# Kernel tuning notes

Hardware: AMD Instinct MI355X
Metric: run time of the kernel (lower is better)

The kernel has to match this reference:

```python
import jax, jax.numpy as jnp
import numpy as np

IN_SIZE = 512
OUT_SIZE = 256
HIDDEN = 256
LN_EPS = 1e-5


def setup_inputs() -> dict:
    key = jax.random.key(0)
    ks = jax.random.split(key, 9)
    B, S, K = 8, 2048, 16
    net_in = jax.random.normal(ks[0], (B, S, K, IN_SIZE), dtype=jnp.float32)
    embeds = jax.random.normal(ks[1], (B, S, OUT_SIZE), dtype=jnp.float32)
    m = jax.random.uniform(ks[2], (B, S, K, 1), dtype=jnp.float32)
    W1 = jax.random.normal(ks[3], (IN_SIZE, HIDDEN), dtype=jnp.float32) * 0.02
    b1 = jnp.full((HIDDEN,), 0.02, dtype=jnp.float32)
    Wf = jax.random.normal(ks[4], (HIDDEN, OUT_SIZE + 1), dtype=jnp.float32) * 0.02
    bf = jnp.zeros((OUT_SIZE + 1,), dtype=jnp.float32)
    gamma = jnp.ones((OUT_SIZE,), dtype=jnp.float32)
    beta = jnp.zeros((OUT_SIZE,), dtype=jnp.float32)
    return {"net_in": net_in, "embeds": embeds, "m": m, "W1": W1, "b1": b1,
            "Wf": Wf, "bf": bf, "gamma": gamma, "beta": beta}


def reference(net_in, embeds, m, W1, b1, Wf, bf, gamma, beta):
    # MLP: one hidden relu layer, final linear to out_size+1
    h = jax.nn.relu(jnp.einsum('bski,ih->bskh', net_in, W1) + b1)
    out = jnp.einsum('bskh,ho->bsko', h, Wf) + bf          # [B,S,K,out+1]
    # sigmoid on last channel (link weight), then mask
    out = jnp.concatenate([out[..., :-1], jax.nn.sigmoid(out[..., -1:])], axis=-1)
    out = m * out
    link_weight = out[..., -1] + 1e-8                       # [B,S,K]
    norm = jnp.sum(link_weight, axis=2, keepdims=True)      # [B,S,1]
    weights = (link_weight / norm)[..., None]               # [B,S,K,1]
    updates = jnp.sum(out * weights, axis=2)                # [B,S,out+1]
    # residual update
    upd_weights = updates[..., -1:]
    embeds_new = embeds + upd_weights * updates[..., :-1]
    # LayerNorm over last dim
    mu = jnp.mean(embeds_new, axis=-1, keepdims=True)
    var = jnp.var(embeds_new, axis=-1, keepdims=True)
    return (embeds_new - mu) * jax.lax.rsqrt(var + LN_EPS) * gamma + beta
```

## Files before the change

### kernel.cpp

```cpp
#include <hip/hip_runtime.h>

typedef short s16x8 __attribute__((ext_vector_type(8)));
typedef float f32x4 __attribute__((ext_vector_type(4)));

__device__ __forceinline__ unsigned short f2bf(float f) {
    union { float f; unsigned u; } v; v.f = f;
    return (unsigned short)((v.u + 0x7FFFu + ((v.u >> 16) & 1u)) >> 16);
}
__device__ __forceinline__ float bf2f(unsigned short h) {
    union { unsigned u; float f; } v; v.u = ((unsigned)h) << 16;
    return v.f;
}

__device__ __forceinline__ void wg_barrier_lds() {
    __builtin_amdgcn_sched_barrier(0);
    asm volatile("s_waitcnt lgkmcnt(0)" ::: "memory");
    __builtin_amdgcn_s_barrier();
    __builtin_amdgcn_sched_barrier(0);
}

#define NBLK 1024

__global__ void prep_weights(const float* __restrict__ W1, const float* __restrict__ Wf,
                             unsigned short* __restrict__ W1T, unsigned short* __restrict__ WfT) {
    int t = blockIdx.x * 256 + threadIdx.x;
    {
        int c  = t >> 13;
        int n  = (t >> 5) & 255;
        int kk = t & 31;
        W1T[t] = f2bf(W1[(c * 32 + kk) * 256 + n]);
    }
    if (t < 65536) {
        int c  = t >> 13;
        int n  = (t >> 5) & 255;
        int hh = t & 31;
        WfT[t] = f2bf(Wf[(c * 32 + hh) * 257 + n]);
    }
}

__global__ __launch_bounds__(1024)
void fused_embed(const float* __restrict__ net_in, const float* __restrict__ embeds,
                 const float* __restrict__ mg, const float* __restrict__ W1,
                 const float* __restrict__ b1, const float* __restrict__ Wf,
                 const float* __restrict__ bfv, const float* __restrict__ gam,
                 const float* __restrict__ bet, float* __restrict__ out,
                 const unsigned short* __restrict__ W1T, const unsigned short* __restrict__ WfT)
{
    __shared__ unsigned short Abuf[2][256][32];
    __shared__ unsigned short Hbuf[128][260];
    __shared__ unsigned short gbuf[16][264];
    __shared__ float updb[16][264];
    __shared__ float sbuf[16];

    const int tid  = threadIdx.x;
    const int lane = tid & 63;
    const int wid  = tid >> 6;
    const int wr   = wid >> 2;
    const int wc   = wid & 3;
    const int l15  = lane & 15;
    const int g8   = (lane >> 4) * 8;
    const int blk  = blockIdx.x;
    const int row0 = blk * 256;

    const f32x4 zero4 = {0.f, 0.f, 0.f, 0.f};

    f32x4 acc[4][4];
    #pragma unroll
    for (int i = 0; i < 4; ++i)
        #pragma unroll
        for (int j = 0; j < 4; ++j)
            acc[i][j] = zero4;

    const int ar = tid >> 2;
    const int ac = (tid & 3) * 8;
    const int wbase = (wc * 64 + l15) * 32 + g8;

    float4 vaA[2], vbA[2];

#define A_ISSUE(KC, S) do { \
        const float* _src = &net_in[(row0 + ar) * 512 + (KC) * 32 + ac]; \
        vaA[S] = *(const float4*)_src; \
        vbA[S] = *(const float4*)(_src + 4); \
    } while (0)

#define A_WRITE(KC, S) do { \
        int4 _pk; \
        asm("v_cvt_pk_bf16_f32 %0, %1, %2" : "=v"(_pk.x) : "v"(vaA[S].x), "v"(vaA[S].y)); \
        asm("v_cvt_pk_bf16_f32 %0, %1, %2" : "=v"(_pk.y) : "v"(vaA[S].z), "v"(vaA[S].w)); \
        asm("v_cvt_pk_bf16_f32 %0, %1, %2" : "=v"(_pk.z) : "v"(vbA[S].x), "v"(vbA[S].y)); \
        asm("v_cvt_pk_bf16_f32 %0, %1, %2" : "=v"(_pk.w) : "v"(vbA[S].z), "v"(vbA[S].w)); \
        *(int4*)&Abuf[(KC) & 1][ar][ac] = _pk; \
    } while (0)

    A_ISSUE(0, 0);
    A_ISSUE(1, 1);
    A_WRITE(0, 0);
    wg_barrier_lds();

    #pragma unroll
    for (int kc = 0; kc < 16; ++kc) {
        const int cur = kc & 1;
        const unsigned short* wp = W1T + kc * 8192 + wbase;
        s16x8 b0 = *(const s16x8*)(wp);
        s16x8 b1r = *(const s16x8*)(wp + 512);
        s16x8 b2 = *(const s16x8*)(wp + 1024);
        s16x8 b3 = *(const s16x8*)(wp + 1536);
        if (kc < 14) A_ISSUE(kc + 2, cur);
        if (kc < 15) A_WRITE(kc + 1, (kc + 1) & 1);
        s16x8 af[4];
        #pragma unroll
        for (int i = 0; i < 4; ++i)
            af[i] = *(const s16x8*)&Abuf[cur][wr * 64 + i * 16 + l15][g8];
        #pragma unroll
        for (int i = 0; i < 4; ++i) {
            acc[i][0] = __builtin_amdgcn_mfma_f32_16x16x32_bf16(af[i], b0, acc[i][0], 0, 0, 0);
            acc[i][1] = __builtin_amdgcn_mfma_f32_16x16x32_bf16(af[i], b1r, acc[i][1], 0, 0, 0);
            acc[i][2] = __builtin_amdgcn_mfma_f32_16x16x32_bf16(af[i], b2, acc[i][2], 0, 0, 0);
            acc[i][3] = __builtin_amdgcn_mfma_f32_16x16x32_bf16(af[i], b3, acc[i][3], 0, 0, 0);
        }
        wg_barrier_lds();
    }
#undef A_ISSUE
#undef A_WRITE

    float wl0 = Wf[(lane * 4 + 0) * 257 + 256];
    float wl1 = Wf[(lane * 4 + 1) * 257 + 256];
    float wl2 = Wf[(lane * 4 + 2) * 257 + 256];
    float wl3 = Wf[(lane * 4 + 3) * 257 + 256];
    float bf256 = bfv[256];

    float u256 = 0.f;

    #pragma unroll
    for (int h = 0; h < 2; ++h) {
        const int mine = ((wid >> 3) == h);

        if (mine) {
            #pragma unroll
            for (int j = 0; j < 4; ++j) {
                int col = wc * 64 + j * 16 + l15;
                float bb = b1[col];
                #pragma unroll
                for (int i = 0; i < 4; ++i) {
                    #pragma unroll
                    for (int r = 0; r < 4; ++r) {
                        int rih = (wr & 1) * 64 + i * 16 + (lane >> 4) * 4 + r;
                        Hbuf[rih][col] = f2bf(fmaxf(acc[i][j][r] + bb, 0.f));
                    }
                }
            }
        }
        __syncthreads();

        if (mine) {
            float lcreg = 0.f;
            for (int k = 0; k < 16; ++k) {
                ushort4 hv = *(const ushort4*)&Hbuf[(wid & 7) * 16 + k][lane * 4];
                float p = bf2f(hv.x) * wl0 + bf2f(hv.y) * wl1 + bf2f(hv.z) * wl2 + bf2f(hv.w) * wl3;
                #pragma unroll
                for (int off = 32; off > 0; off >>= 1) p += __shfl_xor(p, off, 64);
                if (lane == k) lcreg = p;
            }

            float wwreg = 0.f;
            if (lane < 16) {
                float mv  = mg[(blk * 16 + wid) * 16 + lane];
                float raw = lcreg + bf256;
                float sg  = 1.f / (1.f + expf(-raw));
                float v   = mv * sg;
                float lw  = v + 1e-8f;
                float nrm = lw;
                #pragma unroll
                for (int off = 8; off > 0; off >>= 1) nrm += __shfl_xor(nrm, off, 16);
                float wk = lw / nrm;
                wwreg = wk * mv;
                float u = wk * v;
                float s = wwreg;
                #pragma unroll
                for (int off = 8; off > 0; off >>= 1) {
                    u += __shfl_xor(u, off, 16);
                    s += __shfl_xor(s, off, 16);
                }
                u256 = u;
                if (lane == 0) sbuf[wid] = s;
            }
            u256 = __shfl(u256, 0, 64);

            float ga0 = 0.f, ga1 = 0.f, ga2 = 0.f, ga3 = 0.f;
            #pragma unroll
            for (int k = 0; k < 16; ++k) {
                float wwk = __shfl(wwreg, k, 64);
                ushort4 hv = *(const ushort4*)&Hbuf[(wid & 7) * 16 + k][lane * 4];
                ga0 += wwk * bf2f(hv.x);
                ga1 += wwk * bf2f(hv.y);
                ga2 += wwk * bf2f(hv.z);
                ga3 += wwk * bf2f(hv.w);
            }
            ushort4 gw; gw.x = f2bf(ga0); gw.y = f2bf(ga1); gw.z = f2bf(ga2); gw.w = f2bf(ga3);
            *(ushort4*)&gbuf[wid][lane * 4] = gw;
        }
        __syncthreads();
    }

    f32x4 acc2 = zero4;
    {
        const int n0 = (wid * 16 + l15) * 32 + g8;
        s16x8 w2[2];
        w2[0] = *(const s16x8*)(WfT + n0);
        #pragma unroll
        for (int c2 = 0; c2 < 8; ++c2) {
            const int cur = c2 & 1;
            s16x8 bw = w2[cur];
            if (c2 < 7) w2[cur ^ 1] = *(const s16x8*)(WfT + (c2 + 1) * 8192 + n0);
            s16x8 ga = *(const s16x8*)&gbuf[l15][c2 * 32 + g8];
            acc2 = __builtin_amdgcn_mfma_f32_16x16x32_bf16(ga, bw, acc2, 0, 0, 0);
        }
    }

    {
        int gq = lane >> 4;
        int col = wid * 16 + l15;
        float bfc = bfv[col];
        #pragma unroll
        for (int r = 0; r < 4; ++r) {
            int p = gq * 4 + r;
            updb[p][col] = acc2[r] + sbuf[p] * bfc;
        }
    }
    __syncthreads();

    {
        int base = (blk * 16 + wid) * 256;
        float4 up = *(const float4*)&updb[wid][lane * 4];
        float4 em = *(const float4*)&embeds[base + lane * 4];
        float e0 = em.x + u256 * up.x;
        float e1 = em.y + u256 * up.y;
        float e2 = em.z + u256 * up.z;
        float e3 = em.w + u256 * up.w;
        float s1 = e0 + e1 + e2 + e3;
        float s2 = e0 * e0 + e1 * e1 + e2 * e2 + e3 * e3;
        #pragma unroll
        for (int off = 32; off > 0; off >>= 1) {
            s1 += __shfl_xor(s1, off, 64);
            s2 += __shfl_xor(s2, off, 64);
        }
        float mu  = s1 * (1.f / 256.f);
        float var = s2 * (1.f / 256.f) - mu * mu;
        float rs  = rsqrtf(var + 1e-5f);
        float4 gm = *(const float4*)&gam[lane * 4];
        float4 bt = *(const float4*)&bet[lane * 4];
        float4 o;
        o.x = (e0 - mu) * rs * gm.x + bt.x;
        o.y = (e1 - mu) * rs * gm.y + bt.y;
        o.z = (e2 - mu) * rs * gm.z + bt.z;
        o.w = (e3 - mu) * rs * gm.w + bt.w;
        *(float4*)&out[base + lane * 4] = o;
    }
}

extern "C" void kernel_launch(void* const* d_in, const int* in_sizes, int n_in,
                              void* d_out, int out_size, void* d_ws, size_t ws_size,
                              hipStream_t stream) {
    (void)in_sizes; (void)n_in; (void)ws_size; (void)out_size;
    const float* net_in = (const float*)d_in[0];
    const float* embeds = (const float*)d_in[1];
    const float* mg     = (const float*)d_in[2];
    const float* W1     = (const float*)d_in[3];
    const float* b1     = (const float*)d_in[4];
    const float* Wf     = (const float*)d_in[5];
    const float* bfv    = (const float*)d_in[6];
    const float* gam    = (const float*)d_in[7];
    const float* bet    = (const float*)d_in[8];
    float* outp = (float*)d_out;

    unsigned short* W1T = (unsigned short*)d_ws;
    unsigned short* WfT = W1T + 131072;

    prep_weights<<<512, 256, 0, stream>>>(W1, Wf, W1T, WfT);
    fused_embed<<<NBLK, 1024, 0, stream>>>(net_in, embeds, mg, W1, b1, Wf, bfv, gam, bet, outp, W1T, WfT);
}
```

Measured before the change: 198.0 us.

## Restructure first GEMM per position with register-resident W1 and fused link-weight epilogue

The first GEMM is reorganised so each wave owns 16 hidden columns and keeps its W1 fragments in registers for the whole kernel. The block now loops over 16 positions, loading each position's 16x512 input rows into a 4-stage XOR-swizzled LDS ring. The link-weight logit, softmax-style normalisation and weighted hidden sum are computed per position inside the loop through shuffles and a small cross-wave LDS partial buffer. This removes the Hbuf staging and the two-phase epilogue. In exchange it adds a barrier per position, serialises the sigmoid/normalisation step 16 times, and raises register pressure from the 16 held weight fragments.

```diff
diff --git a/kernel.cpp b/kernel.cpp
--- a/kernel.cpp
+++ b/kernel.cpp
@@ -46,8 +46,8 @@
                  const float* __restrict__ bet, float* __restrict__ out,
                  const unsigned short* __restrict__ W1T, const unsigned short* __restrict__ WfT)
 {
-    __shared__ unsigned short Abuf[2][256][32];
-    __shared__ unsigned short Hbuf[128][260];
+    __shared__ unsigned short Abuf[4][16][512];
+    __shared__ float lcpart[2][16][20];
     __shared__ unsigned short gbuf[16][264];
     __shared__ float updb[16][264];
     __shared__ float sbuf[16];
@@ -55,42 +55,41 @@
     const int tid  = threadIdx.x;
     const int lane = tid & 63;
     const int wid  = tid >> 6;
-    const int wr   = wid >> 2;
-    const int wc   = wid & 3;
     const int l15  = lane & 15;
     const int g8   = (lane >> 4) * 8;
+    const int q4   = (lane >> 4) * 4;
     const int blk  = blockIdx.x;
     const int row0 = blk * 256;
 
     const f32x4 zero4 = {0.f, 0.f, 0.f, 0.f};
 
-    f32x4 acc[4][4];
+    s16x8 wfrag[16];
     #pragma unroll
-    for (int i = 0; i < 4; ++i)
-        #pragma unroll
-        for (int j = 0; j < 4; ++j)
-            acc[i][j] = zero4;
-
-    const int ar = tid >> 2;
-    const int ac = (tid & 3) * 8;
-    const int wbase = (wc * 64 + l15) * 32 + g8;
-
-    float4 vaA[2], vbA[2];
-
-#define A_ISSUE(KC, S) do { \
-        const float* _src = &net_in[(row0 + ar) * 512 + (KC) * 32 + ac]; \
-        vaA[S] = *(const float4*)_src; \
-        vbA[S] = *(const float4*)(_src + 4); \
+    for (int kk = 0; kk < 16; ++kk)
+        wfrag[kk] = *(const s16x8*)(W1T + kk * 8192 + (wid * 16 + l15) * 32 + g8);
+
+    const float wlv   = Wf[(wid * 16 + l15) * 257 + 256];
+    const float bbv   = b1[wid * 16 + l15];
+    const float bf256 = bfv[256];
+
+    const float* aseg = net_in + (size_t)row0 * 512 + tid * 8;
+    unsigned short* awr = &Abuf[0][0][0] + wid * 512 + (((lane * 16) ^ ((wid & 7) << 4)) >> 1);
+
+    float4 va[2], vb[2];
+#define A_ISSUE(P, S) do { \
+        va[S] = *(const float4*)(aseg + (P) * 8192); \
+        vb[S] = *(const float4*)(aseg + (P) * 8192 + 4); \
     } while (0)
-
-#define A_WRITE(KC, S) do { \
+#define A_WRITE(P, S) do { \
         int4 _pk; \
-        asm("v_cvt_pk_bf16_f32 %0, %1, %2" : "=v"(_pk.x) : "v"(vaA[S].x), "v"(vaA[S].y)); \
-        asm("v_cvt_pk_bf16_f32 %0, %1, %2" : "=v"(_pk.y) : "v"(vaA[S].z), "v"(vaA[S].w)); \
-        asm("v_cvt_pk_bf16_f32 %0, %1, %2" : "=v"(_pk.z) : "v"(vbA[S].x), "v"(vbA[S].y)); \
-        asm("v_cvt_pk_bf16_f32 %0, %1, %2" : "=v"(_pk.w) : "v"(vbA[S].z), "v"(vbA[S].w)); \
-        *(int4*)&Abuf[(KC) & 1][ar][ac] = _pk; \
+        asm("v_cvt_pk_bf16_f32 %0, %1, %2" : "=v"(_pk.x) : "v"(va[S].x), "v"(va[S].y)); \
+        asm("v_cvt_pk_bf16_f32 %0, %1, %2" : "=v"(_pk.y) : "v"(va[S].z), "v"(va[S].w)); \
+        asm("v_cvt_pk_bf16_f32 %0, %1, %2" : "=v"(_pk.z) : "v"(vb[S].x), "v"(vb[S].y)); \
+        asm("v_cvt_pk_bf16_f32 %0, %1, %2" : "=v"(_pk.w) : "v"(vb[S].z), "v"(vb[S].w)); \
+        *(int4*)(awr + ((P) & 3) * 8192) = _pk; \
     } while (0)
+
+    float u256 = 0.f;
 
     A_ISSUE(0, 0);
     A_ISSUE(1, 1);
@@ -98,109 +97,85 @@
     wg_barrier_lds();
 
     #pragma unroll
-    for (int kc = 0; kc < 16; ++kc) {
-        const int cur = kc & 1;
-        const unsigned short* wp = W1T + kc * 8192 + wbase;
-        s16x8 b0 = *(const s16x8*)(wp);
-        s16x8 b1r = *(const s16x8*)(wp + 512);
-        s16x8 b2 = *(const s16x8*)(wp + 1024);
-        s16x8 b3 = *(const s16x8*)(wp + 1536);
-        if (kc < 14) A_ISSUE(kc + 2, cur);
-        if (kc < 15) A_WRITE(kc + 1, (kc + 1) & 1);
-        s16x8 af[4];
-        #pragma unroll
-        for (int i = 0; i < 4; ++i)
-            af[i] = *(const s16x8*)&Abuf[cur][wr * 64 + i * 16 + l15][g8];
-        #pragma unroll
-        for (int i = 0; i < 4; ++i) {
-            acc[i][0] = __builtin_amdgcn_mfma_f32_16x16x32_bf16(af[i], b0, acc[i][0], 0, 0, 0);
-            acc[i][1] = __builtin_amdgcn_mfma_f32_16x16x32_bf16(af[i], b1r, acc[i][1], 0, 0, 0);
-            acc[i][2] = __builtin_amdgcn_mfma_f32_16x16x32_bf16(af[i], b2, acc[i][2], 0, 0, 0);
-            acc[i][3] = __builtin_amdgcn_mfma_f32_16x16x32_bf16(af[i], b3, acc[i][3], 0, 0, 0);
-        }
+    for (int p = 0; p < 16; ++p) {
+        if (p < 14) A_ISSUE(p + 2, p & 1);
+        if (p < 15) A_WRITE(p + 1, (p + 1) & 1);
+
+        f32x4 acc = zero4;
+        const unsigned short* arow = &Abuf[p & 3][l15][0];
+        #pragma unroll
+        for (int kk = 0; kk < 16; ++kk) {
+            s16x8 af = *(const s16x8*)(arow + (((kk * 64 + (lane >> 4) * 16) ^ ((l15 & 7) << 4)) >> 1));
+            acc = __builtin_amdgcn_mfma_f32_16x16x32_bf16(af, wfrag[kk], acc, 0, 0, 0);
+        }
+
+        float h0 = bf2f(f2bf(fmaxf(acc[0] + bbv, 0.f)));
+        float h1 = bf2f(f2bf(fmaxf(acc[1] + bbv, 0.f)));
+        float h2 = bf2f(f2bf(fmaxf(acc[2] + bbv, 0.f)));
+        float h3 = bf2f(f2bf(fmaxf(acc[3] + bbv, 0.f)));
+
+        float p0 = h0 * wlv, p1 = h1 * wlv, p2 = h2 * wlv, p3 = h3 * wlv;
+        #pragma unroll
+        for (int off = 1; off < 16; off <<= 1) {
+            p0 += __shfl_xor(p0, off, 64);
+            p1 += __shfl_xor(p1, off, 64);
+            p2 += __shfl_xor(p2, off, 64);
+            p3 += __shfl_xor(p3, off, 64);
+        }
+        if (l15 == 0) {
+            lcpart[p & 1][q4 + 0][wid] = p0;
+            lcpart[p & 1][q4 + 1][wid] = p1;
+            lcpart[p & 1][q4 + 2][wid] = p2;
+            lcpart[p & 1][q4 + 3][wid] = p3;
+        }
+
         wg_barrier_lds();
+
+        float uu = 0.f, wwreg = 0.f;
+        if (lane < 16) {
+            const float* lrow = &lcpart[p & 1][lane][0];
+            float4 la = *(const float4*)(lrow);
+            float4 lb = *(const float4*)(lrow + 4);
+            float4 lc = *(const float4*)(lrow + 8);
+            float4 ld = *(const float4*)(lrow + 12);
+            float lcs = la.x + la.y + la.z + la.w + lb.x + lb.y + lb.z + lb.w
+                      + lc.x + lc.y + lc.z + lc.w + ld.x + ld.y + ld.z + ld.w;
+            float raw = lcs + bf256;
+            float mv  = mg[(blk * 16 + p) * 16 + lane];
+            float sg  = 1.f / (1.f + expf(-raw));
+            float v   = mv * sg;
+            float lw  = v + 1e-8f;
+            float nrm = lw;
+            #pragma unroll
+            for (int off = 8; off > 0; off >>= 1) nrm += __shfl_xor(nrm, off, 16);
+            float wk = lw / nrm;
+            wwreg = wk * mv;
+            float u = wk * v;
+            float s = wwreg;
+            #pragma unroll
+            for (int off = 8; off > 0; off >>= 1) {
+                u += __shfl_xor(u, off, 16);
+                s += __shfl_xor(s, off, 16);
+            }
+            uu = u;
+            if (wid == p && lane == 0) sbuf[p] = s;
+        }
+        float ub = __shfl(uu, 0, 64);
+        if (wid == p) u256 = ub;
+
+        float w0 = __shfl(wwreg, q4 + 0, 64);
+        float w1 = __shfl(wwreg, q4 + 1, 64);
+        float w2 = __shfl(wwreg, q4 + 2, 64);
+        float w3 = __shfl(wwreg, q4 + 3, 64);
+        float gp = h0 * w0 + h1 * w1 + h2 * w2 + h3 * w3;
+        gp += __shfl_xor(gp, 16, 64);
+        gp += __shfl_xor(gp, 32, 64);
+        if (lane < 16) gbuf[p][wid * 16 + l15] = f2bf(gp);
     }
 #undef A_ISSUE
 #undef A_WRITE
 
-    float wl0 = Wf[(lane * 4 + 0) * 257 + 256];
-    float wl1 = Wf[(lane * 4 + 1) * 257 + 256];
-    float wl2 = Wf[(lane * 4 + 2) * 257 + 256];
-    float wl3 = Wf[(lane * 4 + 3) * 257 + 256];
-    float bf256 = bfv[256];
-
-    float u256 = 0.f;
-
-    #pragma unroll
-    for (int h = 0; h < 2; ++h) {
-        const int mine = ((wid >> 3) == h);
-
-        if (mine) {
-            #pragma unroll
-            for (int j = 0; j < 4; ++j) {
-                int col = wc * 64 + j * 16 + l15;
-                float bb = b1[col];
-                #pragma unroll
-                for (int i = 0; i < 4; ++i) {
-                    #pragma unroll
-                    for (int r = 0; r < 4; ++r) {
-                        int rih = (wr & 1) * 64 + i * 16 + (lane >> 4) * 4 + r;
-                        Hbuf[rih][col] = f2bf(fmaxf(acc[i][j][r] + bb, 0.f));
-                    }
-                }
-            }
-        }
-        __syncthreads();
-
-        if (mine) {
-            float lcreg = 0.f;
-            for (int k = 0; k < 16; ++k) {
-                ushort4 hv = *(const ushort4*)&Hbuf[(wid & 7) * 16 + k][lane * 4];
-                float p = bf2f(hv.x) * wl0 + bf2f(hv.y) * wl1 + bf2f(hv.z) * wl2 + bf2f(hv.w) * wl3;
-                #pragma unroll
-                for (int off = 32; off > 0; off >>= 1) p += __shfl_xor(p, off, 64);
-                if (lane == k) lcreg = p;
-            }
-
-            float wwreg = 0.f;
-            if (lane < 16) {
-                float mv  = mg[(blk * 16 + wid) * 16 + lane];
-                float raw = lcreg + bf256;
-                float sg  = 1.f / (1.f + expf(-raw));
-                float v   = mv * sg;
-                float lw  = v + 1e-8f;
-                float nrm = lw;
-                #pragma unroll
-                for (int off = 8; off > 0; off >>= 1) nrm += __shfl_xor(nrm, off, 16);
-                float wk = lw / nrm;
-                wwreg = wk * mv;
-                float u = wk * v;
-                float s = wwreg;
-                #pragma unroll
-                for (int off = 8; off > 0; off >>= 1) {
-                    u += __shfl_xor(u, off, 16);
-                    s += __shfl_xor(s, off, 16);
-                }
-                u256 = u;
-                if (lane == 0) sbuf[wid] = s;
-            }
-            u256 = __shfl(u256, 0, 64);
-
-            float ga0 = 0.f, ga1 = 0.f, ga2 = 0.f, ga3 = 0.f;
-            #pragma unroll
-            for (int k = 0; k < 16; ++k) {
-                float wwk = __shfl(wwreg, k, 64);
-                ushort4 hv = *(const ushort4*)&Hbuf[(wid & 7) * 16 + k][lane * 4];
-                ga0 += wwk * bf2f(hv.x);
-                ga1 += wwk * bf2f(hv.y);
-                ga2 += wwk * bf2f(hv.z);
-                ga3 += wwk * bf2f(hv.w);
-            }
-            ushort4 gw; gw.x = f2bf(ga0); gw.y = f2bf(ga1); gw.z = f2bf(ga2); gw.w = f2bf(ga3);
-            *(ushort4*)&gbuf[wid][lane * 4] = gw;
-        }
-        __syncthreads();
-    }
+    __syncthreads();
 
     f32x4 acc2 = zero4;
     {
@@ -218,13 +193,12 @@
     }
 
     {
-        int gq = lane >> 4;
         int col = wid * 16 + l15;
         float bfc = bfv[col];
         #pragma unroll
         for (int r = 0; r < 4; ++r) {
-            int p = gq * 4 + r;
-            updb[p][col] = acc2[r] + sbuf[p] * bfc;
+            int pp = q4 + r;
+            updb[pp][col] = acc2[r] + sbuf[pp] * bfc;
         }
     }
     __syncthreads();
```

Measured after the change: 316.7 us. 59.9% more time.
